# Kernel tuning notes

Hardware: AMD Instinct MI355X
Metric: run time of the kernel (lower is better)

Reference implementation:

```python
import jax, jax.numpy as jnp
import numpy as np

B, H, W = 8, 64, 64
D_MODEL, D_STATE, D_INNER, DT_RANK, K = 96, 16, 192, 6, 4
EPS = 1e-6


def setup_inputs() -> dict:
    key = jax.random.key(0)
    ks = jax.random.split(key, 9)
    f = lambda k, s, sc=0.02: jax.random.normal(k, s, dtype=jnp.float32) * sc
    return {
        "x": jax.random.normal(ks[0], (B, H, W, D_MODEL), jnp.float32),
        "in_proj_w": f(ks[1], (2 * D_INNER, D_MODEL)),
        "conv_w": f(ks[2], (D_INNER, 1, 3, 3), 0.1),
        "conv_b": jnp.zeros((D_INNER,), jnp.float32),
        "x_proj_w": f(ks[3], (K * (DT_RANK + 2 * D_STATE), D_INNER)),
        "dt_projs_w": f(ks[4], (K * D_INNER, DT_RANK), 0.1),
        "A_logs": jnp.log(jax.random.uniform(ks[5], (K * D_INNER, D_STATE), jnp.float32, 1.0, 16.0)),
        "Ds": jnp.ones((K * D_INNER,), jnp.float32),
        "dt_projs_bias": f(ks[6], (K * D_INNER,), 0.5),
        "norm_w": jnp.ones((D_INNER,), jnp.float32),
        "norm_b": jnp.zeros((D_INNER,), jnp.float32),
        "out_proj_w": f(ks[7], (D_MODEL, D_INNER)),
    }


def _ss2d(x, in_proj_w, conv_w, conv_b, x_proj_w, dt_projs_w, A_logs, Ds,
          dt_projs_bias, norm_w, norm_b, out_proj_w):
    silu = jax.nn.silu
    Bb, Hh, Ww, _ = x.shape
    L = Hh * Ww
    # in_proj, split x/z, z gate activation
    xz = x @ in_proj_w.T                                   # (B,H,W,2*Di)
    xx, z = jnp.split(xz, 2, axis=-1)
    z = silu(z)
    # depthwise conv 3x3 in NCHW
    xc = jnp.transpose(xx, (0, 3, 1, 2))                   # (B,Di,H,W)
    xc = jax.lax.conv_general_dilated(
        xc, conv_w, (1, 1), ((1, 1), (1, 1)),
        dimension_numbers=("NCHW", "OIHW", "NCHW"),
        feature_group_count=D_INNER) + conv_b[None, :, None, None]
    xc = silu(xc)
    # 4-way cross scan: hw, wh (transposed), and their reversals
    x_hw = xc.reshape(Bb, D_INNER, L)
    x_wh = jnp.transpose(xc, (0, 1, 3, 2)).reshape(Bb, D_INNER, L)
    xs = jnp.stack([x_hw, x_wh, x_hw[..., ::-1], x_wh[..., ::-1]], axis=1)  # (B,K,Di,L)
    # per-group projections for dt, B, C
    xpw = x_proj_w.reshape(K, DT_RANK + 2 * D_STATE, D_INNER)
    x_dbl = jnp.einsum("bkdl,kcd->bkcl", xs, xpw)
    dts, Bs, Cs = jnp.split(x_dbl, [DT_RANK, DT_RANK + D_STATE], axis=2)
    dtw = dt_projs_w.reshape(K, D_INNER, DT_RANK)
    dts = jnp.einsum("bkrl,kdr->bkdl", dts, dtw)           # (B,K,Di,L)
    A = -jnp.exp(A_logs).reshape(K, D_INNER, D_STATE)      # (K,Di,N)
    dt = jax.nn.softplus(dts + dt_projs_bias.reshape(1, K, D_INNER, 1))
    # selective scan over L
    def step(h, inp):
        u_t, dt_t, B_t, C_t = inp                          # (B,K,Di),(B,K,Di),(B,K,N),(B,K,N)
        dA = jnp.exp(dt_t[..., None] * A)                  # (B,K,Di,N)
        h = h * dA + (dt_t * u_t)[..., None] * B_t[:, :, None, :]
        y = jnp.einsum("bkdn,bkn->bkd", h, C_t)
        return h, y
    h0 = jnp.zeros((Bb, K, D_INNER, D_STATE), jnp.float32)
    seq = (jnp.moveaxis(xs, -1, 0), jnp.moveaxis(dt, -1, 0),
           jnp.moveaxis(Bs, -1, 0), jnp.moveaxis(Cs, -1, 0))
    _, ysL = jax.lax.scan(step, h0, seq)
    ys = jnp.moveaxis(ysL, 0, -1)                          # (B,K,Di,L)
    ys = ys + xs * Ds.reshape(1, K, D_INNER, 1)
    # cross merge: invert flips and wh-transpose, then sum the 4 directions
    y = ys[:, 0] + ys[:, 2][..., ::-1]
    yw = ys[:, 1] + ys[:, 3][..., ::-1]
    y = y + yw.reshape(Bb, D_INNER, Ww, Hh).transpose(0, 1, 3, 2).reshape(Bb, D_INNER, L)
    y = y.reshape(Bb, D_INNER, Hh, Ww).transpose(0, 2, 3, 1)   # (B,H,W,Di)
    # out LayerNorm over channels
    mean = y.mean(-1, keepdims=True)
    var = ((y - mean) ** 2).mean(-1, keepdims=True)
    y = (y - mean) / jnp.sqrt(var + EPS) * norm_w + norm_b
    # gate and out_proj
    y = y * z
    return y @ out_proj_w.T                                # (B,H,W,d_model)


def reference(x, in_proj_w, conv_w, conv_b, x_proj_w, dt_projs_w, A_logs, Ds,
              dt_projs_bias, norm_w, norm_b, out_proj_w):
    return _ss2d(x, in_proj_w, conv_w, conv_b, x_proj_w, dt_projs_w, A_logs, Ds,
                 dt_projs_bias, norm_w, norm_b, out_proj_w)
```

## Files before the change

### kernel.cpp

```cpp
#include <hip/hip_runtime.h>
#include <hip/hip_bf16.h>
#include <math.h>

#define BB 8
#define HS 64
#define WS 64
#define LL 4096
#define DM 96
#define DI 192
#define NS 16
#define RR 6
#define KK 4
#define NCH 64
#define LC 64
#define XP 16
#define EPSN 1e-6f

typedef __attribute__((ext_vector_type(2))) float f32x2;

__device__ __forceinline__ float fsilu(float x) { return x / (1.f + __expf(-x)); }
__device__ __forceinline__ float rexp2(float x) {
    float r; asm("v_exp_f32 %0, %1" : "=v"(r) : "v"(x)); return r;
}
__device__ __forceinline__ float rlog2(float x) {
    float r; asm("v_log_f32 %0, %1" : "=v"(r) : "v"(x)); return r;
}
__device__ __forceinline__ f32x2 pk_mul(f32x2 a, f32x2 b) {
    f32x2 d; asm("v_pk_mul_f32 %0, %1, %2" : "=v"(d) : "v"(a), "v"(b)); return d;
}
__device__ __forceinline__ f32x2 pk_fma(f32x2 a, f32x2 b, f32x2 c) {
    f32x2 d; asm("v_pk_fma_f32 %0, %1, %2, %3" : "=v"(d) : "v"(a), "v"(b), "v"(c)); return d;
}
__device__ __forceinline__ float fsoftplus(float x) {
    float t = rexp2(x * 1.44269504f);
    float r = 0.69314718f * rlog2(1.f + t);
    return (x > 20.f) ? x : r;
}
__device__ __forceinline__ int lmap(int k, int t) {
    int tt = (k >= 2) ? (LL - 1 - t) : t;
    if (k & 1) tt = ((tt & 63) << 6) | (tt >> 6);
    return tt;
}

__global__ __launch_bounds__(384) void k_inproj(const float* __restrict__ x,
        const float* __restrict__ Win, float* __restrict__ xx, float* __restrict__ zs) {
    __shared__ __align__(16) float xrow[8][96];
    int p0 = blockIdx.x * 8;
    int tid = threadIdx.x;
    {
        const float4* src = (const float4*)(x + (size_t)p0 * 96);
        float4* dst = (float4*)&xrow[0][0];
        if (tid < 192) dst[tid] = src[tid];
    }
    __syncthreads();
    const float4* wr4 = (const float4*)(Win + (size_t)tid * 96);
    float acc[8] = {0.f, 0.f, 0.f, 0.f, 0.f, 0.f, 0.f, 0.f};
    #pragma unroll 6
    for (int i = 0; i < 24; ++i) {
        float4 w4 = wr4[i];
        #pragma unroll
        for (int p = 0; p < 8; ++p) {
            float4 x4 = *(const float4*)&xrow[p][i * 4];
            acc[p] += w4.x * x4.x + w4.y * x4.y + w4.z * x4.z + w4.w * x4.w;
        }
    }
    if (tid < DI) {
        #pragma unroll
        for (int p = 0; p < 8; ++p) xx[(size_t)(p0 + p) * DI + tid] = acc[p];
    } else {
        int d = tid - DI;
        #pragma unroll
        for (int p = 0; p < 8; ++p) zs[(size_t)(p0 + p) * DI + d] = fsilu(acc[p]);
    }
}

__global__ __launch_bounds__(256) void k_conv(const float* __restrict__ xx,
        const float* __restrict__ cw, const float* __restrict__ cb,
        const float* __restrict__ Ds, float* __restrict__ xc, float* __restrict__ y0) {
    int idx = blockIdx.x * 256 + threadIdx.x;
    int d = idx % DI; int P = idx / DI;
    int l = P & (LL - 1); int h = l >> 6; int w = l & 63;
    float acc = cb[d];
    #pragma unroll
    for (int i = 0; i < 3; ++i) {
        int hh = h + i - 1;
        if ((unsigned)hh < 64u) {
            #pragma unroll
            for (int j = 0; j < 3; ++j) {
                int ww = w + j - 1;
                if ((unsigned)ww < 64u)
                    acc += xx[(size_t)(P + (i - 1) * 64 + (j - 1)) * DI + d] * cw[d * 9 + i * 3 + j];
            }
        }
    }
    float s = fsilu(acc);
    float sd = Ds[d] + Ds[DI + d] + Ds[2 * DI + d] + Ds[3 * DI + d];
    xc[idx] = s;
    y0[idx] = s * sd;
}

__global__ __launch_bounds__(192) void k_xdbl(const float* __restrict__ xc,
        const float* __restrict__ xpw, float* __restrict__ dts_raw,
        float* __restrict__ Bs, float* __restrict__ Cs) {
    __shared__ __align__(16) float xt[XP][DI];
    int tid = threadIdx.x;
    int p0 = blockIdx.x * XP;
    {
        const float4* src = (const float4*)(xc + (size_t)p0 * DI);
        float4* dst = (float4*)&xt[0][0];
        #pragma unroll
        for (int e = 0; e < XP * DI / 4 / 192; ++e) dst[tid + e * 192] = src[tid + e * 192];
    }
    __syncthreads();
    int c = tid;
    int k = c / 38, c2 = c % 38;
    const float4* w4p = (const float4*)(xpw + (size_t)c * DI);
    float acc[XP];
    #pragma unroll
    for (int p = 0; p < XP; ++p) acc[p] = 0.f;
    if (c < 152) {
        #pragma unroll 4
        for (int i = 0; i < DI / 4; ++i) {
            float4 w4 = w4p[i];
            #pragma unroll
            for (int p = 0; p < XP; ++p) {
                float4 x4 = *(const float4*)&xt[p][i * 4];
                acc[p] += w4.x * x4.x + w4.y * x4.y + w4.z * x4.z + w4.w * x4.w;
            }
        }
        #pragma unroll
        for (int p = 0; p < XP; ++p) {
            int P = p0 + p;
            int b = P >> 12; int l = P & (LL - 1);
            int lt = ((l & 63) << 6) | (l >> 6);
            int tk = (k == 0) ? l : (k == 1) ? lt : (k == 2) ? (LL - 1 - l) : (LL - 1 - lt);
            size_t it = ((size_t)(b * KK + k) * LL + tk);
            if (c2 < RR)            dts_raw[it * RR + c2] = acc[p];
            else if (c2 < RR + NS)  Bs[it * NS + (c2 - RR)] = acc[p];
            else                    Cs[it * NS + (c2 - RR - NS)] = acc[p];
        }
    }
}

__global__ __launch_bounds__(192) void k_scan1(const float* __restrict__ xc,
        const float* __restrict__ dts_raw, const float* __restrict__ Bsg,
        const float* __restrict__ A_logs, const float* __restrict__ dtw,
        const float* __restrict__ dtb,
        float* __restrict__ asum_g, float* __restrict__ hpart) {
    __shared__ __align__(16) float dts_s[LC * 8];
    __shared__ __align__(16) float bs_s[LC * NS];
    int bi = blockIdx.x;
    int b = bi >> 8; int rem = bi & 255; int k = rem >> 6; int c0 = rem & 63;
    int t0 = c0 * LC;
    int d = threadIdx.x;
    size_t g0 = (size_t)(b * KK + k) * LL + t0;
    for (int e = d; e < LC * RR; e += DI) dts_s[(e / RR) * 8 + (e % RR)] = dts_raw[g0 * RR + e];
    for (int e = d; e < LC * NS; e += DI) bs_s[e] = Bsg[g0 * NS + e];
    __syncthreads();
    int kd = k * DI + d;
    f32x2 Ar2v[8];
    #pragma unroll
    for (int n2 = 0; n2 < 8; ++n2) {
        Ar2v[n2].x = -__expf(A_logs[(size_t)kd * NS + 2 * n2]) * 1.44269504f;
        Ar2v[n2].y = -__expf(A_logs[(size_t)kd * NS + 2 * n2 + 1]) * 1.44269504f;
    }
    f32x2 dw2[3];
    #pragma unroll
    for (int r = 0; r < 3; ++r) { dw2[r].x = dtw[kd * RR + 2 * r]; dw2[r].y = dtw[kd * RR + 2 * r + 1]; }
    float bias = dtb[kd];
    f32x2 h2[8];
    #pragma unroll
    for (int n2 = 0; n2 < 8; ++n2) h2[n2] = (f32x2){0.f, 0.f};
    float asum = 0.f;
    const float* xcb = xc + (size_t)b * LL * DI + d;
    float uu[4];
    #pragma unroll
    for (int j = 0; j < 4; ++j) uu[j] = xcb[(size_t)lmap(k, t0 + j) * DI];
    for (int tg = 0; tg < LC; tg += 4) {
        float un[4];
        int tb = t0 + ((tg + 4 < LC) ? (tg + 4) : tg);
        #pragma unroll
        for (int j = 0; j < 4; ++j) un[j] = xcb[(size_t)lmap(k, tb + j) * DI];
        #pragma unroll
        for (int j = 0; j < 4; ++j) {
            int t = tg + j;
            float4 q4 = *(const float4*)&dts_s[t * 8];
            float2 q2 = *(const float2*)&dts_s[t * 8 + 4];
            f32x2 a2 = pk_mul((f32x2){q4.x, q4.y}, dw2[0]);
            a2 = pk_fma((f32x2){q4.z, q4.w}, dw2[1], a2);
            a2 = pk_fma((f32x2){q2.x, q2.y}, dw2[2], a2);
            float dt = fsoftplus(bias + a2.x + a2.y);
            asum += dt;
            float dtu = dt * uu[j];
            f32x2 dt2 = {dt, dt}, dtu2 = {dtu, dtu};
            #pragma unroll
            for (int n4 = 0; n4 < 4; ++n4) {
                float4 b4 = *(const float4*)&bs_s[t * NS + n4 * 4];
                f32x2 tl = pk_mul(dt2, Ar2v[n4 * 2]);
                f32x2 th = pk_mul(dt2, Ar2v[n4 * 2 + 1]);
                f32x2 el = {rexp2(tl.x), rexp2(tl.y)};
                f32x2 eh = {rexp2(th.x), rexp2(th.y)};
                h2[n4 * 2]     = pk_fma(h2[n4 * 2],     el, pk_mul(dtu2, (f32x2){b4.x, b4.y}));
                h2[n4 * 2 + 1] = pk_fma(h2[n4 * 2 + 1], eh, pk_mul(dtu2, (f32x2){b4.z, b4.w}));
            }
        }
        #pragma unroll
        for (int j = 0; j < 4; ++j) uu[j] = un[j];
    }
    asum_g[(size_t)bi * DI + d] = asum;
    size_t base = ((size_t)bi * DI + d) * NS;
    #pragma unroll
    for (int n4 = 0; n4 < 4; ++n4) {
        float4 hv = make_float4(h2[n4 * 2].x, h2[n4 * 2].y, h2[n4 * 2 + 1].x, h2[n4 * 2 + 1].y);
        *(float4*)&hpart[base + n4 * 4] = hv;
    }
}

__global__ __launch_bounds__(256) void k_mid(const float* __restrict__ asum_g,
        const float* __restrict__ A_logs, float* __restrict__ hpp) {
    int g = blockIdx.x * 256 + threadIdx.x;
    int bk = g / (DI * NS);
    int rem = g % (DI * NS);
    int d = rem >> 4; int n = rem & 15;
    int k = bk & 3;
    float Ar2 = -__expf(A_logs[(size_t)(k * DI + d) * NS + n]) * 1.44269504f;
    float h = 0.f;
    for (int c = 0; c < NCH; ++c) {
        size_t row = (size_t)(bk * NCH + c) * DI + d;
        float a = rexp2(Ar2 * asum_g[row]);
        size_t ix = row * NS + n;
        float hp = hpp[ix];
        hpp[ix] = h;
        h = a * h + hp;
    }
}

__global__ __launch_bounds__(192) void k_scan2(const float* __restrict__ xc,
        const float* __restrict__ dts_raw, const float* __restrict__ Bsg,
        const float* __restrict__ Csg, const float* __restrict__ A_logs,
        const float* __restrict__ dtw, const float* __restrict__ dtb,
        const float* __restrict__ hinb, float* __restrict__ y0) {
    __shared__ __align__(16) float dts_s[LC * 8];
    __shared__ __align__(16) float bs_s[LC * NS];
    __shared__ __align__(16) float cs_s[LC * NS];
    int bi = blockIdx.x;
    int b = bi >> 8; int rem = bi & 255; int k = rem >> 6; int c0 = rem & 63;
    int t0 = c0 * LC;
    int d = threadIdx.x;
    size_t g0 = (size_t)(b * KK + k) * LL + t0;
    for (int e = d; e < LC * RR; e += DI) dts_s[(e / RR) * 8 + (e % RR)] = dts_raw[g0 * RR + e];
    for (int e = d; e < LC * NS; e += DI) bs_s[e] = Bsg[g0 * NS + e];
    for (int e = d; e < LC * NS; e += DI) cs_s[e] = Csg[g0 * NS + e];
    __syncthreads();
    int kd = k * DI + d;
    f32x2 Ar2v[8];
    #pragma unroll
    for (int n2 = 0; n2 < 8; ++n2) {
        Ar2v[n2].x = -__expf(A_logs[(size_t)kd * NS + 2 * n2]) * 1.44269504f;
        Ar2v[n2].y = -__expf(A_logs[(size_t)kd * NS + 2 * n2 + 1]) * 1.44269504f;
    }
    f32x2 dw2[3];
    #pragma unroll
    for (int r = 0; r < 3; ++r) { dw2[r].x = dtw[kd * RR + 2 * r]; dw2[r].y = dtw[kd * RR + 2 * r + 1]; }
    float bias = dtb[kd];
    size_t base = ((size_t)bi * DI + d) * NS;
    f32x2 h2[8];
    #pragma unroll
    for (int n4 = 0; n4 < 4; ++n4) {
        float4 hv = *(const float4*)&hinb[base + n4 * 4];
        h2[n4 * 2]     = (f32x2){hv.x, hv.y};
        h2[n4 * 2 + 1] = (f32x2){hv.z, hv.w};
    }
    const float* xcb = xc + (size_t)b * LL * DI + d;
    float* y0b = y0 + (size_t)b * LL * DI + d;
    float uu[4];
    #pragma unroll
    for (int j = 0; j < 4; ++j) uu[j] = xcb[(size_t)lmap(k, t0 + j) * DI];
    for (int tg = 0; tg < LC; tg += 4) {
        float un[4];
        int tb = t0 + ((tg + 4 < LC) ? (tg + 4) : tg);
        #pragma unroll
        for (int j = 0; j < 4; ++j) un[j] = xcb[(size_t)lmap(k, tb + j) * DI];
        #pragma unroll
        for (int j = 0; j < 4; ++j) {
            int t = tg + j;
            int lx = lmap(k, t0 + t);
            float4 q4 = *(const float4*)&dts_s[t * 8];
            float2 q2 = *(const float2*)&dts_s[t * 8 + 4];
            f32x2 a2 = pk_mul((f32x2){q4.x, q4.y}, dw2[0]);
            a2 = pk_fma((f32x2){q4.z, q4.w}, dw2[1], a2);
            a2 = pk_fma((f32x2){q2.x, q2.y}, dw2[2], a2);
            float dt = fsoftplus(bias + a2.x + a2.y);
            float dtu = dt * uu[j];
            f32x2 dt2 = {dt, dt}, dtu2 = {dtu, dtu};
            f32x2 y2 = {0.f, 0.f};
            #pragma unroll
            for (int n4 = 0; n4 < 4; ++n4) {
                float4 b4 = *(const float4*)&bs_s[t * NS + n4 * 4];
                float4 c4 = *(const float4*)&cs_s[t * NS + n4 * 4];
                f32x2 tl = pk_mul(dt2, Ar2v[n4 * 2]);
                f32x2 th = pk_mul(dt2, Ar2v[n4 * 2 + 1]);
                f32x2 el = {rexp2(tl.x), rexp2(tl.y)};
                f32x2 eh = {rexp2(th.x), rexp2(th.y)};
                h2[n4 * 2]     = pk_fma(h2[n4 * 2],     el, pk_mul(dtu2, (f32x2){b4.x, b4.y}));
                h2[n4 * 2 + 1] = pk_fma(h2[n4 * 2 + 1], eh, pk_mul(dtu2, (f32x2){b4.z, b4.w}));
                y2 = pk_fma(h2[n4 * 2],     (f32x2){c4.x, c4.y}, y2);
                y2 = pk_fma(h2[n4 * 2 + 1], (f32x2){c4.z, c4.w}, y2);
            }
            atomicAdd(&y0b[(size_t)lx * DI], y2.x + y2.y);
        }
        #pragma unroll
        for (int j = 0; j < 4; ++j) uu[j] = un[j];
    }
}

__global__ __launch_bounds__(256) void k_final(const float* __restrict__ y0,
        const float* __restrict__ zs, const float* __restrict__ nw,
        const float* __restrict__ nb, const float* __restrict__ Wout,
        float* __restrict__ out) {
    __shared__ __align__(16) float gs[32][DI];
    int tid = threadIdx.x;
    int wv = tid >> 6, lane = tid & 63;
    int Pbase = blockIdx.x * 32;
    float nwv[3], nbv[3];
    #pragma unroll
    for (int j = 0; j < 3; ++j) { nwv[j] = nw[lane + 64 * j]; nbv[j] = nb[lane + 64 * j]; }
    for (int pi = 0; pi < 8; ++pi) {
        int pl = wv * 8 + pi;
        size_t Poff = (size_t)(Pbase + pl) * DI;
        float v[3];
        #pragma unroll
        for (int j = 0; j < 3; ++j) v[j] = y0[Poff + lane + 64 * j];
        float s = v[0] + v[1] + v[2];
        #pragma unroll
        for (int o = 32; o; o >>= 1) s += __shfl_xor(s, o);
        float mean = s * (1.f / 192.f);
        float ss = 0.f;
        #pragma unroll
        for (int j = 0; j < 3; ++j) { float dd = v[j] - mean; ss += dd * dd; }
        #pragma unroll
        for (int o = 32; o; o >>= 1) ss += __shfl_xor(ss, o);
        float rstd = rsqrtf(ss * (1.f / 192.f) + EPSN);
        #pragma unroll
        for (int j = 0; j < 3; ++j) {
            int c = lane + 64 * j;
            gs[pl][c] = ((v[j] - mean) * rstd * nwv[j] + nbv[j]) * zs[Poff + c];
        }
    }
    __syncthreads();
    int o = tid & 127;
    int pg = tid >> 7;
    if (o < DM) {
        const float* wr = Wout + (size_t)o * DI;
        float acc[16];
        #pragma unroll
        for (int p = 0; p < 16; ++p) acc[p] = 0.f;
        for (int k0 = 0; k0 < DI; k0 += 4) {
            float4 w4 = *(const float4*)(wr + k0);
            #pragma unroll
            for (int p = 0; p < 16; ++p) {
                float4 g4 = *(const float4*)(&gs[pg * 16 + p][k0]);
                acc[p] += w4.x * g4.x + w4.y * g4.y + w4.z * g4.z + w4.w * g4.w;
            }
        }
        #pragma unroll
        for (int p = 0; p < 16; ++p)
            out[(size_t)(Pbase + pg * 16 + p) * DM + o] = acc[p];
    }
}

extern "C" void kernel_launch(void* const* d_in, const int* in_sizes, int n_in,
                              void* d_out, int out_size, void* d_ws, size_t ws_size,
                              hipStream_t stream) {
    const float* x      = (const float*)d_in[0];
    const float* in_w   = (const float*)d_in[1];
    const float* conv_w = (const float*)d_in[2];
    const float* conv_b = (const float*)d_in[3];
    const float* xpw    = (const float*)d_in[4];
    const float* dtw    = (const float*)d_in[5];
    const float* A_logs = (const float*)d_in[6];
    const float* Ds     = (const float*)d_in[7];
    const float* dtb    = (const float*)d_in[8];
    const float* nw     = (const float*)d_in[9];
    const float* nb     = (const float*)d_in[10];
    const float* out_w  = (const float*)d_in[11];
    float* out = (float*)d_out;

    char* ws = (char*)d_ws;
    size_t off = 0;
    auto alloc = [&](size_t n) { float* p = (float*)(ws + off); off += n * sizeof(float); return p; };
    float* xx   = alloc((size_t)BB * LL * DI);
    float* zs   = alloc((size_t)BB * LL * DI);
    float* xc   = alloc((size_t)BB * LL * DI);
    float* y0   = alloc((size_t)BB * LL * DI);
    float* dts  = alloc((size_t)BB * KK * LL * RR);
    float* Bsb  = alloc((size_t)BB * KK * LL * NS);
    float* Csb  = alloc((size_t)BB * KK * LL * NS);
    float* asum = alloc((size_t)BB * KK * NCH * DI);
    float* hpp  = alloc((size_t)BB * KK * NCH * DI * NS);

    k_inproj<<<BB * LL / 8, 384, 0, stream>>>(x, in_w, xx, zs);
    k_conv<<<BB * LL * DI / 256, 256, 0, stream>>>(xx, conv_w, conv_b, Ds, xc, y0);
    k_xdbl<<<BB * LL / XP, 192, 0, stream>>>(xc, xpw, dts, Bsb, Csb);
    k_scan1<<<BB * KK * NCH, DI, 0, stream>>>(xc, dts, Bsb, A_logs, dtw, dtb, asum, hpp);
    k_mid<<<(BB * KK * DI * NS) / 256, 256, 0, stream>>>(asum, A_logs, hpp);
    k_scan2<<<BB * KK * NCH, DI, 0, stream>>>(xc, dts, Bsb, Csb, A_logs, dtw, dtb, hpp, y0);
    k_final<<<BB * LL / 32, 256, 0, stream>>>(y0, zs, nw, nb, out_w, out);
}
```

Baseline: 443.5 us.

## Process two channels per thread and two chunks per block in scan kernels

Each block of 192 threads in both scan kernels now covers two consecutive time chunks. Each thread handles two channels (d and d+96) for one chunk, so the block grid is halved. The goal is more independent instruction-level parallelism per thread, two interleaved recurrences that hide exp and FMA latency, with the shared dt and B/C loads reused across both channels. The cost is roughly doubled register pressure, which may lower occupancy, and fewer blocks to fill the GPU.

```diff
diff --git a/kernel.cpp b/kernel.cpp
--- a/kernel.cpp
+++ b/kernel.cpp
@@ -147,72 +147,99 @@
         const float* __restrict__ A_logs, const float* __restrict__ dtw,
         const float* __restrict__ dtb,
         float* __restrict__ asum_g, float* __restrict__ hpart) {
-    __shared__ __align__(16) float dts_s[LC * 8];
-    __shared__ __align__(16) float bs_s[LC * NS];
+    __shared__ __align__(16) float dts_s[2 * LC * 8];
+    __shared__ __align__(16) float bs_s[2 * LC * NS];
     int bi = blockIdx.x;
-    int b = bi >> 8; int rem = bi & 255; int k = rem >> 6; int c0 = rem & 63;
-    int t0 = c0 * LC;
-    int d = threadIdx.x;
-    size_t g0 = (size_t)(b * KK + k) * LL + t0;
-    for (int e = d; e < LC * RR; e += DI) dts_s[(e / RR) * 8 + (e % RR)] = dts_raw[g0 * RR + e];
-    for (int e = d; e < LC * NS; e += DI) bs_s[e] = Bsg[g0 * NS + e];
+    int b = bi >> 7; int rem = bi & 127; int k = rem >> 5; int cp = rem & 31;
+    int tid = threadIdx.x;
+    size_t g0 = (size_t)(b * KK + k) * LL + cp * 2 * LC;
+    for (int e = tid; e < 2 * LC * RR; e += 192) dts_s[(e / RR) * 8 + (e % RR)] = dts_raw[g0 * RR + e];
+    for (int e = tid; e < 2 * LC * NS; e += 192) bs_s[e] = Bsg[g0 * NS + e];
     __syncthreads();
-    int kd = k * DI + d;
-    f32x2 Ar2v[8];
+    int ch = tid / 96;
+    int d0 = tid % 96;
+    int c = cp * 2 + ch;
+    int t0 = c * LC;
+    int tl0 = ch * LC;
+    int kd0 = k * DI + d0, kd1 = kd0 + 96;
+    f32x2 Ara[8], Arb[8];
     #pragma unroll
     for (int n2 = 0; n2 < 8; ++n2) {
-        Ar2v[n2].x = -__expf(A_logs[(size_t)kd * NS + 2 * n2]) * 1.44269504f;
-        Ar2v[n2].y = -__expf(A_logs[(size_t)kd * NS + 2 * n2 + 1]) * 1.44269504f;
-    }
-    f32x2 dw2[3];
-    #pragma unroll
-    for (int r = 0; r < 3; ++r) { dw2[r].x = dtw[kd * RR + 2 * r]; dw2[r].y = dtw[kd * RR + 2 * r + 1]; }
-    float bias = dtb[kd];
-    f32x2 h2[8];
-    #pragma unroll
-    for (int n2 = 0; n2 < 8; ++n2) h2[n2] = (f32x2){0.f, 0.f};
-    float asum = 0.f;
-    const float* xcb = xc + (size_t)b * LL * DI + d;
-    float uu[4];
-    #pragma unroll
-    for (int j = 0; j < 4; ++j) uu[j] = xcb[(size_t)lmap(k, t0 + j) * DI];
+        Ara[n2].x = -__expf(A_logs[(size_t)kd0 * NS + 2 * n2]) * 1.44269504f;
+        Ara[n2].y = -__expf(A_logs[(size_t)kd0 * NS + 2 * n2 + 1]) * 1.44269504f;
+        Arb[n2].x = -__expf(A_logs[(size_t)kd1 * NS + 2 * n2]) * 1.44269504f;
+        Arb[n2].y = -__expf(A_logs[(size_t)kd1 * NS + 2 * n2 + 1]) * 1.44269504f;
+    }
+    f32x2 dwa[3], dwb[3];
+    #pragma unroll
+    for (int r = 0; r < 3; ++r) {
+        dwa[r].x = dtw[kd0 * RR + 2 * r]; dwa[r].y = dtw[kd0 * RR + 2 * r + 1];
+        dwb[r].x = dtw[kd1 * RR + 2 * r]; dwb[r].y = dtw[kd1 * RR + 2 * r + 1];
+    }
+    float bias0 = dtb[kd0], bias1 = dtb[kd1];
+    f32x2 ha[8], hb[8];
+    #pragma unroll
+    for (int n2 = 0; n2 < 8; ++n2) { ha[n2] = (f32x2){0.f, 0.f}; hb[n2] = (f32x2){0.f, 0.f}; }
+    float asum0 = 0.f, asum1 = 0.f;
+    const float* xcb = xc + (size_t)b * LL * DI + d0;
+    float uu[2][4];
+    #pragma unroll
+    for (int j = 0; j < 4; ++j) {
+        size_t o = (size_t)lmap(k, t0 + j) * DI;
+        uu[0][j] = xcb[o]; uu[1][j] = xcb[o + 96];
+    }
     for (int tg = 0; tg < LC; tg += 4) {
-        float un[4];
+        float un[2][4];
         int tb = t0 + ((tg + 4 < LC) ? (tg + 4) : tg);
         #pragma unroll
-        for (int j = 0; j < 4; ++j) un[j] = xcb[(size_t)lmap(k, tb + j) * DI];
+        for (int j = 0; j < 4; ++j) {
+            size_t o = (size_t)lmap(k, tb + j) * DI;
+            un[0][j] = xcb[o]; un[1][j] = xcb[o + 96];
+        }
         #pragma unroll
         for (int j = 0; j < 4; ++j) {
             int t = tg + j;
-            float4 q4 = *(const float4*)&dts_s[t * 8];
-            float2 q2 = *(const float2*)&dts_s[t * 8 + 4];
-            f32x2 a2 = pk_mul((f32x2){q4.x, q4.y}, dw2[0]);
-            a2 = pk_fma((f32x2){q4.z, q4.w}, dw2[1], a2);
-            a2 = pk_fma((f32x2){q2.x, q2.y}, dw2[2], a2);
-            float dt = fsoftplus(bias + a2.x + a2.y);
-            asum += dt;
-            float dtu = dt * uu[j];
-            f32x2 dt2 = {dt, dt}, dtu2 = {dtu, dtu};
+            float4 q4 = *(const float4*)&dts_s[(tl0 + t) * 8];
+            float2 q2 = *(const float2*)&dts_s[(tl0 + t) * 8 + 4];
+            f32x2 p01 = {q4.x, q4.y}, p23 = {q4.z, q4.w}, p45 = {q2.x, q2.y};
+            f32x2 aa = pk_fma(p45, dwa[2], pk_fma(p23, dwa[1], pk_mul(p01, dwa[0])));
+            f32x2 ab = pk_fma(p45, dwb[2], pk_fma(p23, dwb[1], pk_mul(p01, dwb[0])));
+            float dt0 = fsoftplus(bias0 + aa.x + aa.y);
+            float dt1 = fsoftplus(bias1 + ab.x + ab.y);
+            asum0 += dt0; asum1 += dt1;
+            float dtu0 = dt0 * uu[0][j], dtu1 = dt1 * uu[1][j];
+            f32x2 dt0v = {dt0, dt0}, dt1v = {dt1, dt1};
+            f32x2 du0v = {dtu0, dtu0}, du1v = {dtu1, dtu1};
             #pragma unroll
             for (int n4 = 0; n4 < 4; ++n4) {
-                float4 b4 = *(const float4*)&bs_s[t * NS + n4 * 4];
-                f32x2 tl = pk_mul(dt2, Ar2v[n4 * 2]);
-                f32x2 th = pk_mul(dt2, Ar2v[n4 * 2 + 1]);
-                f32x2 el = {rexp2(tl.x), rexp2(tl.y)};
-                f32x2 eh = {rexp2(th.x), rexp2(th.y)};
-                h2[n4 * 2]     = pk_fma(h2[n4 * 2],     el, pk_mul(dtu2, (f32x2){b4.x, b4.y}));
-                h2[n4 * 2 + 1] = pk_fma(h2[n4 * 2 + 1], eh, pk_mul(dtu2, (f32x2){b4.z, b4.w}));
+                float4 b4 = *(const float4*)&bs_s[(tl0 + t) * NS + n4 * 4];
+                f32x2 blo = {b4.x, b4.y}, bhi = {b4.z, b4.w};
+                f32x2 tla = pk_mul(dt0v, Ara[n4 * 2]);
+                f32x2 tha = pk_mul(dt0v, Ara[n4 * 2 + 1]);
+                f32x2 ela = {rexp2(tla.x), rexp2(tla.y)};
+                f32x2 eha = {rexp2(tha.x), rexp2(tha.y)};
+                ha[n4 * 2]     = pk_fma(ha[n4 * 2],     ela, pk_mul(du0v, blo));
+                ha[n4 * 2 + 1] = pk_fma(ha[n4 * 2 + 1], eha, pk_mul(du0v, bhi));
+                f32x2 tlb = pk_mul(dt1v, Arb[n4 * 2]);
+                f32x2 thb = pk_mul(dt1v, Arb[n4 * 2 + 1]);
+                f32x2 elb = {rexp2(tlb.x), rexp2(tlb.y)};
+                f32x2 ehb = {rexp2(thb.x), rexp2(thb.y)};
+                hb[n4 * 2]     = pk_fma(hb[n4 * 2],     elb, pk_mul(du1v, blo));
+                hb[n4 * 2 + 1] = pk_fma(hb[n4 * 2 + 1], ehb, pk_mul(du1v, bhi));
             }
         }
         #pragma unroll
-        for (int j = 0; j < 4; ++j) uu[j] = un[j];
-    }
-    asum_g[(size_t)bi * DI + d] = asum;
-    size_t base = ((size_t)bi * DI + d) * NS;
+        for (int j = 0; j < 4; ++j) { uu[0][j] = un[0][j]; uu[1][j] = un[1][j]; }
+    }
+    int bic = (b * KK + k) * NCH + c;
+    asum_g[(size_t)bic * DI + d0] = asum0;
+    asum_g[(size_t)bic * DI + d0 + 96] = asum1;
+    size_t base0 = ((size_t)bic * DI + d0) * NS;
+    size_t base1 = base0 + (size_t)96 * NS;
     #pragma unroll
     for (int n4 = 0; n4 < 4; ++n4) {
-        float4 hv = make_float4(h2[n4 * 2].x, h2[n4 * 2].y, h2[n4 * 2 + 1].x, h2[n4 * 2 + 1].y);
-        *(float4*)&hpart[base + n4 * 4] = hv;
+        *(float4*)&hpart[base0 + n4 * 4] = make_float4(ha[n4*2].x, ha[n4*2].y, ha[n4*2+1].x, ha[n4*2+1].y);
+        *(float4*)&hpart[base1 + n4 * 4] = make_float4(hb[n4*2].x, hb[n4*2].y, hb[n4*2+1].x, hb[n4*2+1].y);
     }
 }
 
@@ -240,77 +267,108 @@
         const float* __restrict__ Csg, const float* __restrict__ A_logs,
         const float* __restrict__ dtw, const float* __restrict__ dtb,
         const float* __restrict__ hinb, float* __restrict__ y0) {
-    __shared__ __align__(16) float dts_s[LC * 8];
-    __shared__ __align__(16) float bs_s[LC * NS];
-    __shared__ __align__(16) float cs_s[LC * NS];
+    __shared__ __align__(16) float dts_s[2 * LC * 8];
+    __shared__ __align__(16) float bs_s[2 * LC * NS];
+    __shared__ __align__(16) float cs_s[2 * LC * NS];
     int bi = blockIdx.x;
-    int b = bi >> 8; int rem = bi & 255; int k = rem >> 6; int c0 = rem & 63;
-    int t0 = c0 * LC;
-    int d = threadIdx.x;
-    size_t g0 = (size_t)(b * KK + k) * LL + t0;
-    for (int e = d; e < LC * RR; e += DI) dts_s[(e / RR) * 8 + (e % RR)] = dts_raw[g0 * RR + e];
-    for (int e = d; e < LC * NS; e += DI) bs_s[e] = Bsg[g0 * NS + e];
-    for (int e = d; e < LC * NS; e += DI) cs_s[e] = Csg[g0 * NS + e];
+    int b = bi >> 7; int rem = bi & 127; int k = rem >> 5; int cp = rem & 31;
+    int tid = threadIdx.x;
+    size_t g0 = (size_t)(b * KK + k) * LL + cp * 2 * LC;
+    for (int e = tid; e < 2 * LC * RR; e += 192) dts_s[(e / RR) * 8 + (e % RR)] = dts_raw[g0 * RR + e];
+    for (int e = tid; e < 2 * LC * NS; e += 192) bs_s[e] = Bsg[g0 * NS + e];
+    for (int e = tid; e < 2 * LC * NS; e += 192) cs_s[e] = Csg[g0 * NS + e];
     __syncthreads();
-    int kd = k * DI + d;
-    f32x2 Ar2v[8];
+    int ch = tid / 96;
+    int d0 = tid % 96;
+    int c = cp * 2 + ch;
+    int t0 = c * LC;
+    int tl0 = ch * LC;
+    int kd0 = k * DI + d0, kd1 = kd0 + 96;
+    f32x2 Ara[8], Arb[8];
     #pragma unroll
     for (int n2 = 0; n2 < 8; ++n2) {
-        Ar2v[n2].x = -__expf(A_logs[(size_t)kd * NS + 2 * n2]) * 1.44269504f;
-        Ar2v[n2].y = -__expf(A_logs[(size_t)kd * NS + 2 * n2 + 1]) * 1.44269504f;
-    }
-    f32x2 dw2[3];
-    #pragma unroll
-    for (int r = 0; r < 3; ++r) { dw2[r].x = dtw[kd * RR + 2 * r]; dw2[r].y = dtw[kd * RR + 2 * r + 1]; }
-    float bias = dtb[kd];
-    size_t base = ((size_t)bi * DI + d) * NS;
-    f32x2 h2[8];
+        Ara[n2].x = -__expf(A_logs[(size_t)kd0 * NS + 2 * n2]) * 1.44269504f;
+        Ara[n2].y = -__expf(A_logs[(size_t)kd0 * NS + 2 * n2 + 1]) * 1.44269504f;
+        Arb[n2].x = -__expf(A_logs[(size_t)kd1 * NS + 2 * n2]) * 1.44269504f;
+        Arb[n2].y = -__expf(A_logs[(size_t)kd1 * NS + 2 * n2 + 1]) * 1.44269504f;
+    }
+    f32x2 dwa[3], dwb[3];
+    #pragma unroll
+    for (int r = 0; r < 3; ++r) {
+        dwa[r].x = dtw[kd0 * RR + 2 * r]; dwa[r].y = dtw[kd0 * RR + 2 * r + 1];
+        dwb[r].x = dtw[kd1 * RR + 2 * r]; dwb[r].y = dtw[kd1 * RR + 2 * r + 1];
+    }
+    float bias0 = dtb[kd0], bias1 = dtb[kd1];
+    int bic = (b * KK + k) * NCH + c;
+    size_t base0 = ((size_t)bic * DI + d0) * NS;
+    size_t base1 = base0 + (size_t)96 * NS;
+    f32x2 ha[8], hb[8];
     #pragma unroll
     for (int n4 = 0; n4 < 4; ++n4) {
-        float4 hv = *(const float4*)&hinb[base + n4 * 4];
-        h2[n4 * 2]     = (f32x2){hv.x, hv.y};
-        h2[n4 * 2 + 1] = (f32x2){hv.z, hv.w};
-    }
-    const float* xcb = xc + (size_t)b * LL * DI + d;
-    float* y0b = y0 + (size_t)b * LL * DI + d;
-    float uu[4];
-    #pragma unroll
-    for (int j = 0; j < 4; ++j) uu[j] = xcb[(size_t)lmap(k, t0 + j) * DI];
+        float4 hv = *(const float4*)&hinb[base0 + n4 * 4];
+        ha[n4 * 2] = (f32x2){hv.x, hv.y}; ha[n4 * 2 + 1] = (f32x2){hv.z, hv.w};
+        float4 hw = *(const float4*)&hinb[base1 + n4 * 4];
+        hb[n4 * 2] = (f32x2){hw.x, hw.y}; hb[n4 * 2 + 1] = (f32x2){hw.z, hw.w};
+    }
+    const float* xcb = xc + (size_t)b * LL * DI + d0;
+    float* y0b = y0 + (size_t)b * LL * DI + d0;
+    float uu[2][4];
+    #pragma unroll
+    for (int j = 0; j < 4; ++j) {
+        size_t o = (size_t)lmap(k, t0 + j) * DI;
+        uu[0][j] = xcb[o]; uu[1][j] = xcb[o + 96];
+    }
     for (int tg = 0; tg < LC; tg += 4) {
-        float un[4];
+        float un[2][4];
         int tb = t0 + ((tg + 4 < LC) ? (tg + 4) : tg);
         #pragma unroll
-        for (int j = 0; j < 4; ++j) un[j] = xcb[(size_t)lmap(k, tb + j) * DI];
+        for (int j = 0; j < 4; ++j) {
+            size_t o = (size_t)lmap(k, tb + j) * DI;
+            un[0][j] = xcb[o]; un[1][j] = xcb[o + 96];
+        }
         #pragma unroll
         for (int j = 0; j < 4; ++j) {
             int t = tg + j;
             int lx = lmap(k, t0 + t);
-            float4 q4 = *(const float4*)&dts_s[t * 8];
-            float2 q2 = *(const float2*)&dts_s[t * 8 + 4];
-            f32x2 a2 = pk_mul((f32x2){q4.x, q4.y}, dw2[0]);
-            a2 = pk_fma((f32x2){q4.z, q4.w}, dw2[1], a2);
-            a2 = pk_fma((f32x2){q2.x, q2.y}, dw2[2], a2);
-            float dt = fsoftplus(bias + a2.x + a2.y);
-            float dtu = dt * uu[j];
-            f32x2 dt2 = {dt, dt}, dtu2 = {dtu, dtu};
-            f32x2 y2 = {0.f, 0.f};
+            float4 q4 = *(const float4*)&dts_s[(tl0 + t) * 8];
+            float2 q2 = *(const float2*)&dts_s[(tl0 + t) * 8 + 4];
+            f32x2 p01 = {q4.x, q4.y}, p23 = {q4.z, q4.w}, p45 = {q2.x, q2.y};
+            f32x2 aa = pk_fma(p45, dwa[2], pk_fma(p23, dwa[1], pk_mul(p01, dwa[0])));
+            f32x2 ab = pk_fma(p45, dwb[2], pk_fma(p23, dwb[1], pk_mul(p01, dwb[0])));
+            float dt0 = fsoftplus(bias0 + aa.x + aa.y);
+            float dt1 = fsoftplus(bias1 + ab.x + ab.y);
+            float dtu0 = dt0 * uu[0][j], dtu1 = dt1 * uu[1][j];
+            f32x2 dt0v = {dt0, dt0}, dt1v = {dt1, dt1};
+            f32x2 du0v = {dtu0, dtu0}, du1v = {dtu1, dtu1};
+            f32x2 ya = {0.f, 0.f}, yb = {0.f, 0.f};
             #pragma unroll
             for (int n4 = 0; n4 < 4; ++n4) {
-                float4 b4 = *(const float4*)&bs_s[t * NS + n4 * 4];
-                float4 c4 = *(const float4*)&cs_s[t * NS + n4 * 4];
-                f32x2 tl = pk_mul(dt2, Ar2v[n4 * 2]);
-                f32x2 th = pk_mul(dt2, Ar2v[n4 * 2 + 1]);
-                f32x2 el = {rexp2(tl.x), rexp2(tl.y)};
-                f32x2 eh = {rexp2(th.x), rexp2(th.y)};
-                h2[n4 * 2]     = pk_fma(h2[n4 * 2],     el, pk_mul(dtu2, (f32x2){b4.x, b4.y}));
-                h2[n4 * 2 + 1] = pk_fma(h2[n4 * 2 + 1], eh, pk_mul(dtu2, (f32x2){b4.z, b4.w}));
-                y2 = pk_fma(h2[n4 * 2],     (f32x2){c4.x, c4.y}, y2);
-                y2 = pk_fma(h2[n4 * 2 + 1], (f32x2){c4.z, c4.w}, y2);
+                float4 b4 = *(const float4*)&bs_s[(tl0 + t) * NS + n4 * 4];
+                float4 c4 = *(const float4*)&cs_s[(tl0 + t) * NS + n4 * 4];
+                f32x2 blo = {b4.x, b4.y}, bhi = {b4.z, b4.w};
+                f32x2 clo = {c4.x, c4.y}, chi = {c4.z, c4.w};
+                f32x2 tla = pk_mul(dt0v, Ara[n4 * 2]);
+                f32x2 tha = pk_mul(dt0v, Ara[n4 * 2 + 1]);
+                f32x2 ela = {rexp2(tla.x), rexp2(tla.y)};
+                f32x2 eha = {rexp2(tha.x), rexp2(tha.y)};
+                ha[n4 * 2]     = pk_fma(ha[n4 * 2],     ela, pk_mul(du0v, blo));
+                ha[n4 * 2 + 1] = pk_fma(ha[n4 * 2 + 1], eha, pk_mul(du0v, bhi));
+                ya = pk_fma(ha[n4 * 2], clo, ya);
+                ya = pk_fma(ha[n4 * 2 + 1], chi, ya);
+                f32x2 tlb = pk_mul(dt1v, Arb[n4 * 2]);
+                f32x2 thb = pk_mul(dt1v, Arb[n4 * 2 + 1]);
+                f32x2 elb = {rexp2(tlb.x), rexp2(tlb.y)};
+                f32x2 ehb = {rexp2(thb.x), rexp2(thb.y)};
+                hb[n4 * 2]     = pk_fma(hb[n4 * 2],     elb, pk_mul(du1v, blo));
+                hb[n4 * 2 + 1] = pk_fma(hb[n4 * 2 + 1], ehb, pk_mul(du1v, bhi));
+                yb = pk_fma(hb[n4 * 2], clo, yb);
+                yb = pk_fma(hb[n4 * 2 + 1], chi, yb);
             }
-            atomicAdd(&y0b[(size_t)lx * DI], y2.x + y2.y);
-        }
-        #pragma unroll
-        for (int j = 0; j < 4; ++j) uu[j] = un[j];
+            atomicAdd(&y0b[(size_t)lx * DI], ya.x + ya.y);
+            atomicAdd(&y0b[(size_t)lx * DI + 96], yb.x + yb.y);
+        }
+        #pragma unroll
+        for (int j = 0; j < 4; ++j) { uu[0][j] = un[0][j]; uu[1][j] = un[1][j]; }
     }
 }
 
@@ -402,8 +460,8 @@
     k_inproj<<<BB * LL / 8, 384, 0, stream>>>(x, in_w, xx, zs);
     k_conv<<<BB * LL * DI / 256, 256, 0, stream>>>(xx, conv_w, conv_b, Ds, xc, y0);
     k_xdbl<<<BB * LL / XP, 192, 0, stream>>>(xc, xpw, dts, Bsb, Csb);
-    k_scan1<<<BB * KK * NCH, DI, 0, stream>>>(xc, dts, Bsb, A_logs, dtw, dtb, asum, hpp);
+    k_scan1<<<BB * KK * NCH / 2, 192, 0, stream>>>(xc, dts, Bsb, A_logs, dtw, dtb, asum, hpp);
     k_mid<<<(BB * KK * DI * NS) / 256, 256, 0, stream>>>(asum, A_logs, hpp);
-    k_scan2<<<BB * KK * NCH, DI, 0, stream>>>(xc, dts, Bsb, Csb, A_logs, dtw, dtb, hpp, y0);
+    k_scan2<<<BB * KK * NCH / 2, 192, 0, stream>>>(xc, dts, Bsb, Csb, A_logs, dtw, dtb, hpp, y0);
     k_final<<<BB * LL / 32, 256, 0, stream>>>(y0, zs, nw, nb, out_w, out);
 }
```

Result: no change. 438.1 us (-1.2%).

## Replace scan atomics with per-direction output buffers merged in final kernel

Applied to the files above, without the earlier changes.

The second scan pass now writes each direction's outputs with plain stores into a per-direction buffer instead of atomically adding into a shared y0 array at scattered positions. The final kernel gathers the four direction results via lmap, adds the D-skip term computed from xc, and then applies the layer norm. This removes atomic contention and read-modify-write traffic. In exchange it adds a 4x larger intermediate buffer and four scattered reads per element in the final kernel. The xx buffer aliases the new buffer to limit workspace use.

```diff
diff --git a/kernel.cpp b/kernel.cpp
--- a/kernel.cpp
+++ b/kernel.cpp
@@ -76,7 +76,7 @@
 
 __global__ __launch_bounds__(256) void k_conv(const float* __restrict__ xx,
         const float* __restrict__ cw, const float* __restrict__ cb,
-        const float* __restrict__ Ds, float* __restrict__ xc, float* __restrict__ y0) {
+        float* __restrict__ xc) {
     int idx = blockIdx.x * 256 + threadIdx.x;
     int d = idx % DI; int P = idx / DI;
     int l = P & (LL - 1); int h = l >> 6; int w = l & 63;
@@ -93,10 +93,7 @@
             }
         }
     }
-    float s = fsilu(acc);
-    float sd = Ds[d] + Ds[DI + d] + Ds[2 * DI + d] + Ds[3 * DI + d];
-    xc[idx] = s;
-    y0[idx] = s * sd;
+    xc[idx] = fsilu(acc);
 }
 
 __global__ __launch_bounds__(192) void k_xdbl(const float* __restrict__ xc,
@@ -239,7 +236,7 @@
         const float* __restrict__ dts_raw, const float* __restrict__ Bsg,
         const float* __restrict__ Csg, const float* __restrict__ A_logs,
         const float* __restrict__ dtw, const float* __restrict__ dtb,
-        const float* __restrict__ hinb, float* __restrict__ y0) {
+        const float* __restrict__ hinb, float* __restrict__ ysb) {
     __shared__ __align__(16) float dts_s[LC * 8];
     __shared__ __align__(16) float bs_s[LC * NS];
     __shared__ __align__(16) float cs_s[LC * NS];
@@ -272,7 +269,7 @@
         h2[n4 * 2 + 1] = (f32x2){hv.z, hv.w};
     }
     const float* xcb = xc + (size_t)b * LL * DI + d;
-    float* y0b = y0 + (size_t)b * LL * DI + d;
+    float* ysw = ysb + g0 * DI + d;
     float uu[4];
     #pragma unroll
     for (int j = 0; j < 4; ++j) uu[j] = xcb[(size_t)lmap(k, t0 + j) * DI];
@@ -284,7 +281,6 @@
         #pragma unroll
         for (int j = 0; j < 4; ++j) {
             int t = tg + j;
-            int lx = lmap(k, t0 + t);
             float4 q4 = *(const float4*)&dts_s[t * 8];
             float2 q2 = *(const float2*)&dts_s[t * 8 + 4];
             f32x2 a2 = pk_mul((f32x2){q4.x, q4.y}, dw2[0]);
@@ -307,14 +303,15 @@
                 y2 = pk_fma(h2[n4 * 2],     (f32x2){c4.x, c4.y}, y2);
                 y2 = pk_fma(h2[n4 * 2 + 1], (f32x2){c4.z, c4.w}, y2);
             }
-            atomicAdd(&y0b[(size_t)lx * DI], y2.x + y2.y);
+            ysw[(size_t)t * DI] = y2.x + y2.y;
         }
         #pragma unroll
         for (int j = 0; j < 4; ++j) uu[j] = un[j];
     }
 }
 
-__global__ __launch_bounds__(256) void k_final(const float* __restrict__ y0,
+__global__ __launch_bounds__(256) void k_final(const float* __restrict__ xc,
+        const float* __restrict__ ysb, const float* __restrict__ Ds,
         const float* __restrict__ zs, const float* __restrict__ nw,
         const float* __restrict__ nb, const float* __restrict__ Wout,
         float* __restrict__ out) {
@@ -322,15 +319,29 @@
     int tid = threadIdx.x;
     int wv = tid >> 6, lane = tid & 63;
     int Pbase = blockIdx.x * 32;
-    float nwv[3], nbv[3];
-    #pragma unroll
-    for (int j = 0; j < 3; ++j) { nwv[j] = nw[lane + 64 * j]; nbv[j] = nb[lane + 64 * j]; }
+    float nwv[3], nbv[3], sdv[3];
+    #pragma unroll
+    for (int j = 0; j < 3; ++j) {
+        int c = lane + 64 * j;
+        nwv[j] = nw[c]; nbv[j] = nb[c];
+        sdv[j] = Ds[c] + Ds[DI + c] + Ds[2 * DI + c] + Ds[3 * DI + c];
+    }
     for (int pi = 0; pi < 8; ++pi) {
         int pl = wv * 8 + pi;
-        size_t Poff = (size_t)(Pbase + pl) * DI;
+        int P = Pbase + pl;
+        int b = P >> 12, l = P & (LL - 1);
+        size_t Poff = (size_t)P * DI;
+        size_t r0 = ((size_t)(b * KK + 0) * LL + lmap(0, l)) * DI;
+        size_t r1 = ((size_t)(b * KK + 1) * LL + lmap(1, l)) * DI;
+        size_t r2 = ((size_t)(b * KK + 2) * LL + lmap(2, l)) * DI;
+        size_t r3 = ((size_t)(b * KK + 3) * LL + lmap(3, l)) * DI;
         float v[3];
         #pragma unroll
-        for (int j = 0; j < 3; ++j) v[j] = y0[Poff + lane + 64 * j];
+        for (int j = 0; j < 3; ++j) {
+            int c = lane + 64 * j;
+            v[j] = xc[Poff + c] * sdv[j]
+                 + ysb[r0 + c] + ysb[r1 + c] + ysb[r2 + c] + ysb[r3 + c];
+        }
         float s = v[0] + v[1] + v[2];
         #pragma unroll
         for (int o = 32; o; o >>= 1) s += __shfl_xor(s, o);
@@ -389,21 +400,21 @@
     char* ws = (char*)d_ws;
     size_t off = 0;
     auto alloc = [&](size_t n) { float* p = (float*)(ws + off); off += n * sizeof(float); return p; };
-    float* xx   = alloc((size_t)BB * LL * DI);
     float* zs   = alloc((size_t)BB * LL * DI);
     float* xc   = alloc((size_t)BB * LL * DI);
-    float* y0   = alloc((size_t)BB * LL * DI);
     float* dts  = alloc((size_t)BB * KK * LL * RR);
     float* Bsb  = alloc((size_t)BB * KK * LL * NS);
     float* Csb  = alloc((size_t)BB * KK * LL * NS);
     float* asum = alloc((size_t)BB * KK * NCH * DI);
     float* hpp  = alloc((size_t)BB * KK * NCH * DI * NS);
+    float* ysb  = alloc((size_t)BB * KK * LL * DI);
+    float* xx   = ysb;
 
     k_inproj<<<BB * LL / 8, 384, 0, stream>>>(x, in_w, xx, zs);
-    k_conv<<<BB * LL * DI / 256, 256, 0, stream>>>(xx, conv_w, conv_b, Ds, xc, y0);
+    k_conv<<<BB * LL * DI / 256, 256, 0, stream>>>(xx, conv_w, conv_b, xc);
     k_xdbl<<<BB * LL / XP, 192, 0, stream>>>(xc, xpw, dts, Bsb, Csb);
     k_scan1<<<BB * KK * NCH, DI, 0, stream>>>(xc, dts, Bsb, A_logs, dtw, dtb, asum, hpp);
     k_mid<<<(BB * KK * DI * NS) / 256, 256, 0, stream>>>(asum, A_logs, hpp);
-    k_scan2<<<BB * KK * NCH, DI, 0, stream>>>(xc, dts, Bsb, Csb, A_logs, dtw, dtb, hpp, y0);
-    k_final<<<BB * LL / 32, 256, 0, stream>>>(y0, zs, nw, nb, out_w, out);
-}
+    k_scan2<<<BB * KK * NCH, DI, 0, stream>>>(xc, dts, Bsb, Csb, A_logs, dtw, dtb, hpp, ysb);
+    k_final<<<BB * LL / 32, 256, 0, stream>>>(xc, ysb, Ds, zs, nw, nb, out_w, out);
+}
```

Result: no change. 439.4 us (-0.9%).
